# Kernel optimization log

Hardware: AMD Instinct MI355X
Metric: run time of the kernel (lower is better)

## Reference

```python
import jax, jax.numpy as jnp
import numpy as np
import math

CHANNELS = 512
N_HEADS = 8
K_CH = CHANNELS // N_HEADS            # 64 per-head dim
ROPE_D = int(K_CH * 0.5)              # 32 dims get RoPE, rest pass through
BASE = 10000


def _rope(x):
    # x: [b, h, t, dk]; rotate first ROPE_D dims (half-split style, matching the torch module)
    d = ROPE_D
    t = x.shape[2]
    theta = 1.0 / (BASE ** (jnp.arange(0, d, 2, dtype=jnp.float32) / d))      # [d/2]
    ang = jnp.arange(t, dtype=jnp.float32)[:, None] * theta[None, :]          # [t, d/2]
    ang = jnp.concatenate([ang, ang], axis=-1)                                # [t, d]
    cos = jnp.cos(ang)[None, None, :, :].astype(x.dtype)
    sin = jnp.sin(ang)[None, None, :, :].astype(x.dtype)
    x_rope, x_pass = x[..., :d], x[..., d:]
    neg_half = jnp.concatenate([-x_rope[..., d // 2:], x_rope[..., :d // 2]], axis=-1)
    return jnp.concatenate([x_rope * cos + neg_half * sin, x_pass], axis=-1)


def _split_heads(y):
    # [b, (h c), t] -> [b, h, t, c]
    b, _, t = y.shape
    return y.reshape(b, N_HEADS, K_CH, t).transpose(0, 1, 3, 2)


def setup_inputs() -> dict:
    key = jax.random.key(0)
    ks = jax.random.split(key, 10)
    B, T = 8, 1024
    w_scale = 1.0 / math.sqrt(CHANNELS)
    return {
        "x": jax.random.normal(ks[0], (B, CHANNELS, T), jnp.float32),
        "c": jax.random.normal(ks[1], (B, CHANNELS, T), jnp.float32),
        "Wq": jax.random.normal(ks[2], (CHANNELS, CHANNELS), jnp.float32) * w_scale,
        "bq": jax.random.normal(ks[3], (CHANNELS,), jnp.float32) * 0.02,
        "Wk": jax.random.normal(ks[4], (CHANNELS, CHANNELS), jnp.float32) * w_scale,
        "bk": jax.random.normal(ks[5], (CHANNELS,), jnp.float32) * 0.02,
        "Wv": jax.random.normal(ks[6], (CHANNELS, CHANNELS), jnp.float32) * w_scale,
        "bv": jax.random.normal(ks[7], (CHANNELS,), jnp.float32) * 0.02,
        "Wo": jax.random.normal(ks[8], (CHANNELS, CHANNELS), jnp.float32) * w_scale,
        "bo": jax.random.normal(ks[9], (CHANNELS,), jnp.float32) * 0.02,
    }


def reference(x, c, Wq, bq, Wk, bk, Wv, bv, Wo, bo):
    # 1x1 Conv1d == per-timestep linear over channels
    q = jnp.einsum('oc,bct->bot', Wq, x) + bq[None, :, None]
    k = jnp.einsum('oc,bct->bot', Wk, c) + bk[None, :, None]
    v = jnp.einsum('oc,bct->bot', Wv, c) + bv[None, :, None]

    q = _rope(_split_heads(q))            # [b,h,t,ck]
    k = _rope(_split_heads(k))            # [b,h,s,ck]
    v = _split_heads(v)                   # [b,h,s,ck]

    scale = 1.0 / math.sqrt(K_CH)
    scores = jnp.einsum('bhtc,bhsc->bhts', q, k) * scale
    p_attn = jax.nn.softmax(scores, axis=-1)       # dropout p=0 -> identity
    out = jnp.einsum('bhts,bhsc->bhtc', p_attn, v)

    b, _, t, _ = out.shape
    out = out.transpose(0, 1, 3, 2).reshape(b, CHANNELS, t)   # [b, (h c), t]
    return jnp.einsum('oc,bct->bot', Wo, out) + bo[None, :, None]
```

## Files before the change

kernel.cpp:

```cpp
#include <hip/hip_runtime.h>

typedef __bf16 bf16x8 __attribute__((ext_vector_type(8)));
typedef float  f32x4  __attribute__((ext_vector_type(4)));

__device__ __forceinline__ unsigned short f2bf(float f){
    union { float f; unsigned u; } v; v.f = f;
    v.u += 0x7fffu + ((v.u >> 16) & 1u);
    return (unsigned short)(v.u >> 16);
}
__device__ __forceinline__ unsigned short f2bf_trunc(float f){
    union { float f; unsigned u; } v; v.f = f;
    return (unsigned short)(v.u >> 16);
}
__device__ __forceinline__ void gl2lds16(const unsigned short* g, unsigned short* l){
    __builtin_amdgcn_global_load_lds(
        (const __attribute__((address_space(1))) void*)g,
        (__attribute__((address_space(3))) void*)l, 16, 0, 0);
}

__global__ __launch_bounds__(256) void transpose_cvt(const float* __restrict__ x, const float* __restrict__ c,
                                                     const float* __restrict__ w0, const float* __restrict__ w1,
                                                     const float* __restrict__ w2, const float* __restrict__ w3,
                                                     unsigned short* __restrict__ xt, unsigned short* __restrict__ ct,
                                                     unsigned short* __restrict__ o0, unsigned short* __restrict__ o1,
                                                     unsigned short* __restrict__ o2, unsigned short* __restrict__ o3){
    __shared__ float tile[64][72];
    const int z = blockIdx.z;
    if (z == 16){
        int fid = (blockIdx.x * 8 + blockIdx.y) * 256 + threadIdx.x;
        const float* in; unsigned short* out;
        switch (fid >> 13){
            case 0: in = w0; out = o0; break;
            case 1: in = w1; out = o1; break;
            case 2: in = w2; out = o2; break;
            default: in = w3; out = o3; break;
        }
        int off = (fid & 8191) * 32;
        #pragma unroll
        for (int j = 0; j < 8; j++){
            float4 v = *(const float4*)(in + off + j*4);
            ushort4 o; o.x = f2bf(v.x); o.y = f2bf(v.y); o.z = f2bf(v.z); o.w = f2bf(v.w);
            *(ushort4*)(out + off + j*4) = o;
        }
        return;
    }
    const float* in = (z < 8) ? x : c;
    unsigned short* out = (z < 8) ? xt : ct;
    const int b = z & 7;
    const int t0 = blockIdx.x * 64, c0 = blockIdx.y * 64;
    const int tid = threadIdx.x;
    {
        int r = tid >> 2, q = (tid & 3) * 16;
        const float* src = in + ((size_t)b * 512 + c0 + r) * 1024 + t0 + q;
        #pragma unroll
        for (int j = 0; j < 4; j++)
            *(float4*)&tile[r][q + j*4] = ((const float4*)src)[j];
    }
    __syncthreads();
    {
        int tr = tid >> 2, cj = (tid & 3) * 16;
        unsigned pw[8];
        #pragma unroll
        for (int j = 0; j < 8; j++){
            unsigned lo = f2bf(tile[cj + 2*j    ][tr]);
            unsigned hi = f2bf(tile[cj + 2*j + 1][tr]);
            pw[j] = lo | (hi << 16);
        }
        unsigned short* dst = out + ((size_t)b * 1024 + t0 + tr) * 512 + c0 + cj;
        uint4 q0 = {pw[0], pw[1], pw[2], pw[3]};
        uint4 q1 = {pw[4], pw[5], pw[6], pw[7]};
        ((uint4*)dst)[0] = q0;
        ((uint4*)dst)[1] = q1;
    }
}

__device__ __forceinline__ void gemm_mainloop(const unsigned short* __restrict__ A,
                                              const unsigned short* __restrict__ Bm,
                                              unsigned short* a_s, unsigned short* b_s,
                                              int m0, int n0, int tid, f32x4 acc[4][4]){
    const int wave = tid >> 6, lane = tid & 63;
    const int l15 = lane & 15, l4 = lane >> 4;
    const int mw = (wave >> 1) * 64, nw = (wave & 1) * 64;
    const int r8 = lane >> 3, c8l = lane & 7;
    const int csw = (c8l ^ r8) * 8;
    const int rp = l15 & 7;

    for (int k0 = 0; k0 < 512; k0 += 64){
        #pragma unroll
        for (int i = 0; i < 4; i++){
            int rg = i * 4 + wave;
            int row = rg * 8 + r8;
            gl2lds16(A  + (size_t)(m0 + row) * 512 + k0 + csw, a_s + rg * 512);
            gl2lds16(Bm + (size_t)(n0 + row) * 512 + k0 + csw, b_s + rg * 512);
        }
        __syncthreads();
        #pragma unroll
        for (int kk = 0; kk < 2; kk++){
            bf16x8 af[4], bfr[4];
            #pragma unroll
            for (int mt = 0; mt < 4; mt++)
                af[mt] = *(const bf16x8*)&a_s[(mw + mt*16 + l15)*64 + (((kk*4) + l4) ^ rp)*8];
            #pragma unroll
            for (int ct = 0; ct < 4; ct++)
                bfr[ct] = *(const bf16x8*)&b_s[(nw + ct*16 + l15)*64 + (((kk*4) + l4) ^ rp)*8];
            #pragma unroll
            for (int mt = 0; mt < 4; mt++)
                #pragma unroll
                for (int ct = 0; ct < 4; ct++)
                    acc[mt][ct] = __builtin_amdgcn_mfma_f32_16x16x32_bf16(
                        af[mt], bfr[ct], acc[mt][ct], 0, 0, 0);
        }
        __syncthreads();
    }
}

__global__ __launch_bounds__(256) void qkv_gemm(const unsigned short* __restrict__ xt,
                                                const unsigned short* __restrict__ ct,
                                                const unsigned short* __restrict__ wq,
                                                const unsigned short* __restrict__ wk,
                                                const unsigned short* __restrict__ wv,
                                                const float* __restrict__ bq_,
                                                const float* __restrict__ bk_,
                                                const float* __restrict__ bv_,
                                                unsigned short* __restrict__ qt,
                                                unsigned short* __restrict__ kt,
                                                unsigned short* __restrict__ vct){
    __shared__ unsigned short a_s[128*64];
    __shared__ unsigned short b_s[128*64];
    const int z = blockIdx.y, bid = blockIdx.x;
    const unsigned short *A, *Bm;
    int m0, n0;
    if (z == 0){ A = xt; Bm = wq; m0 = (bid >> 2)*128; n0 = (bid & 3)*128; }
    else if (z == 1){ A = ct; Bm = wk; m0 = (bid >> 2)*128; n0 = (bid & 3)*128; }
    else { A = wv; Bm = ct; m0 = (bid & 3)*128; n0 = (bid >> 2)*128; }
    const int tid = threadIdx.x;
    const int wave = tid >> 6, lane = tid & 63;
    const int l15 = lane & 15, l4 = lane >> 4;
    const int mw = (wave >> 1) * 64, nw = (wave & 1) * 64;
    const f32x4 vzero = {0.f, 0.f, 0.f, 0.f};
    f32x4 acc[4][4];
    #pragma unroll
    for (int i = 0; i < 4; i++)
        #pragma unroll
        for (int j = 0; j < 4; j++) acc[i][j] = vzero;

    gemm_mainloop(A, Bm, a_s, b_s, m0, n0, tid, acc);

    if (z < 2){
        unsigned short* out = (z == 0) ? qt : kt;
        const float* bias = (z == 0) ? bq_ : bk_;
        const float osc = (z == 0) ? 0.1803368801111137f : 1.0f;
        float bv4[4];
        #pragma unroll
        for (int ct2 = 0; ct2 < 4; ct2++) bv4[ct2] = bias[n0 + nw + ct2*16 + l15];
        const float theta = __powf(10000.0f, -(float)l15 * (1.0f / 16.0f));
        #pragma unroll
        for (int mt = 0; mt < 4; mt++){
            #pragma unroll
            for (int rr = 0; rr < 4; rr++){
                int row = m0 + mw + mt*16 + l4*4 + rr;
                int t = row & 1023;
                float v[4];
                #pragma unroll
                for (int ct2 = 0; ct2 < 4; ct2++) v[ct2] = acc[mt][ct2][rr] + bv4[ct2];
                float sn, cn;
                __sincosf((float)t * theta, &sn, &cn);
                float r0 = v[0] * cn - v[1] * sn;
                float r1 = v[1] * cn + v[0] * sn;
                v[0] = r0; v[1] = r1;
                #pragma unroll
                for (int ct2 = 0; ct2 < 4; ct2++)
                    out[(size_t)row * 512 + n0 + nw + ct2*16 + l15] = f2bf(v[ct2] * osc);
            }
        }
    } else {
        #pragma unroll
        for (int mt = 0; mt < 4; mt++){
            #pragma unroll
            for (int rr = 0; rr < 4; rr++){
                int row = m0 + mw + mt*16 + l4*4 + rr;
                float bb = bv_[row];
                #pragma unroll
                for (int ct2 = 0; ct2 < 4; ct2++){
                    int n = n0 + nw + ct2*16 + l15;
                    size_t oaddr = (size_t)(n >> 10) * 524288 + (size_t)row * 1024 + (n & 1023);
                    vct[oaddr] = f2bf(acc[mt][ct2][rr] + bb);
                }
            }
        }
    }
}

__global__ __launch_bounds__(256) void gemm_o(const unsigned short* __restrict__ wo,
                                              const unsigned short* __restrict__ attnT,
                                              const float* __restrict__ bo,
                                              float* __restrict__ out){
    __shared__ unsigned short a_s[64*64];
    __shared__ unsigned short b_s[128*64];
    const int m0 = blockIdx.x * 64, n0 = blockIdx.y * 128;
    const int tid = threadIdx.x;
    const int wave = tid >> 6, lane = tid & 63;
    const int l15 = lane & 15, l4 = lane >> 4;
    const int nw = wave * 32;
    const int r8 = lane >> 3, c8l = lane & 7;
    const int csw = (c8l ^ r8) * 8;
    const int rp = l15 & 7;
    const f32x4 vzero = {0.f, 0.f, 0.f, 0.f};
    f32x4 acc[4][2];
    #pragma unroll
    for (int i = 0; i < 4; i++){ acc[i][0] = vzero; acc[i][1] = vzero; }

    for (int k0 = 0; k0 < 512; k0 += 64){
        #pragma unroll
        for (int i = 0; i < 2; i++){
            int rg = wave * 2 + i;
            gl2lds16(wo + (size_t)(m0 + rg*8 + r8) * 512 + k0 + csw, a_s + rg * 512);
        }
        #pragma unroll
        for (int i = 0; i < 4; i++){
            int rg = wave * 4 + i;
            gl2lds16(attnT + (size_t)(n0 + rg*8 + r8) * 512 + k0 + csw, b_s + rg * 512);
        }
        __syncthreads();
        #pragma unroll
        for (int kk = 0; kk < 2; kk++){
            bf16x8 af[4], bfr[2];
            #pragma unroll
            for (int mt = 0; mt < 4; mt++)
                af[mt] = *(const bf16x8*)&a_s[(mt*16 + l15)*64 + (((kk*4) + l4) ^ rp)*8];
            #pragma unroll
            for (int ct = 0; ct < 2; ct++)
                bfr[ct] = *(const bf16x8*)&b_s[(nw + ct*16 + l15)*64 + (((kk*4) + l4) ^ rp)*8];
            #pragma unroll
            for (int mt = 0; mt < 4; mt++)
                #pragma unroll
                for (int ct = 0; ct < 2; ct++)
                    acc[mt][ct] = __builtin_amdgcn_mfma_f32_16x16x32_bf16(
                        af[mt], bfr[ct], acc[mt][ct], 0, 0, 0);
        }
        __syncthreads();
    }

    #pragma unroll
    for (int mt = 0; mt < 4; mt++){
        #pragma unroll
        for (int rr = 0; rr < 4; rr++){
            int row = m0 + mt*16 + l4*4 + rr;
            float bb = bo[row];
            #pragma unroll
            for (int ct2 = 0; ct2 < 2; ct2++){
                int n = n0 + nw + ct2*16 + l15;
                size_t oaddr = (size_t)(n >> 10) * 524288 + (size_t)row * 1024 + (n & 1023);
                out[oaddr] = acc[mt][ct2][rr] + bb;
            }
        }
    }
}

__global__ __launch_bounds__(256, 2) void flash_attn(const unsigned short* __restrict__ qt,
                                                     const unsigned short* __restrict__ kt,
                                                     const unsigned short* __restrict__ vct,
                                                     unsigned short* __restrict__ attnT){
    __shared__ unsigned short k_s[2][64*64];
    __shared__ unsigned short v_s[2][64*64];
    __shared__ unsigned short p_s[4][16*72];
    const int bhq = blockIdx.x;
    const int bh = bhq & 63, b = bh >> 3, h = bh & 7;
    const int q0 = (bhq >> 6) * 128;
    const int tid = threadIdx.x, wave = tid >> 6, lane = tid & 63;
    const int l15 = lane & 15, l4 = lane >> 4;
    const int r8 = lane >> 3, c8l = lane & 7;
    const int csw = (c8l ^ r8) * 8;
    const int rp = l15 & 7;
    const f32x4 vzero = {0.f, 0.f, 0.f, 0.f};
    const unsigned short* kbase = kt  + (size_t)(b*1024)*512 + h*64;
    const unsigned short* vbase = vct + (size_t)(b*512 + h*64)*1024;

    bf16x8 qf[2][2];
    #pragma unroll
    for (int st = 0; st < 2; st++)
        #pragma unroll
        for (int kh = 0; kh < 2; kh++)
            qf[st][kh] = *(const bf16x8*)(qt + (size_t)(b*1024 + q0 + wave*32 + st*16 + l15)*512
                                             + h*64 + kh*32 + l4*8);
    f32x4 o_acc[2][4], l_acc[2];
    #pragma unroll
    for (int st = 0; st < 2; st++){
        l_acc[st] = vzero;
        #pragma unroll
        for (int dt = 0; dt < 4; dt++) o_acc[st][dt] = vzero;
    }
    const __bf16 one_bf = (__bf16)1.0f;
    const bf16x8 ones = {one_bf, one_bf, one_bf, one_bf, one_bf, one_bf, one_bf, one_bf};

    auto stage = [&](int tile, int buf){
        const int s0n = tile * 64;
        #pragma unroll
        for (int i = 0; i < 2; i++){
            int rg = i * 4 + wave;
            int row = rg * 8 + r8;
            gl2lds16(kbase + (size_t)(s0n + row)*512 + csw, &k_s[buf][rg*512]);
            gl2lds16(vbase + (size_t)row*1024 + s0n + csw, &v_s[buf][rg*512]);
        }
    };
    stage(0, 0);
    __syncthreads();

    for (int it = 0; it < 16; ++it){
        const int cur = it & 1;
        if (it < 15) stage(it + 1, cur ^ 1);
        bf16x8 kf[2][4], vf[2][4];
        #pragma unroll
        for (int kh = 0; kh < 2; kh++)
            #pragma unroll
            for (int ct = 0; ct < 4; ct++)
                kf[kh][ct] = *(const bf16x8*)&k_s[cur][(ct*16 + l15)*64 + ((kh*4 + l4) ^ rp)*8];
        #pragma unroll
        for (int sh = 0; sh < 2; sh++)
            #pragma unroll
            for (int dt = 0; dt < 4; dt++)
                vf[sh][dt] = *(const bf16x8*)&v_s[cur][(dt*16 + l15)*64 + ((sh*4 + l4) ^ rp)*8];
        #pragma unroll
        for (int st = 0; st < 2; st++){
            f32x4 sa[4];
            #pragma unroll
            for (int ct = 0; ct < 4; ct++) sa[ct] = vzero;
            #pragma unroll
            for (int kh = 0; kh < 2; kh++)
                #pragma unroll
                for (int ct = 0; ct < 4; ct++)
                    sa[ct] = __builtin_amdgcn_mfma_f32_16x16x32_bf16(qf[st][kh], kf[kh][ct], sa[ct], 0, 0, 0);
            #pragma unroll
            for (int ct = 0; ct < 4; ct++)
                #pragma unroll
                for (int rr = 0; rr < 4; rr++)
                    sa[ct][rr] = exp2f(sa[ct][rr]);
            #pragma unroll
            for (int ct = 0; ct < 4; ct++)
                #pragma unroll
                for (int rr = 0; rr < 4; rr++)
                    p_s[wave][(l4*4 + rr)*72 + ct*16 + l15] = f2bf_trunc(sa[ct][rr]);
            bf16x8 ap0 = *(const bf16x8*)&p_s[wave][l15*72 + l4*8];
            bf16x8 ap1 = *(const bf16x8*)&p_s[wave][l15*72 + 32 + l4*8];
            l_acc[st] = __builtin_amdgcn_mfma_f32_16x16x32_bf16(ap0, ones, l_acc[st], 0, 0, 0);
            l_acc[st] = __builtin_amdgcn_mfma_f32_16x16x32_bf16(ap1, ones, l_acc[st], 0, 0, 0);
            #pragma unroll
            for (int dt = 0; dt < 4; dt++){
                o_acc[st][dt] = __builtin_amdgcn_mfma_f32_16x16x32_bf16(ap0, vf[0][dt], o_acc[st][dt], 0, 0, 0);
                o_acc[st][dt] = __builtin_amdgcn_mfma_f32_16x16x32_bf16(ap1, vf[1][dt], o_acc[st][dt], 0, 0, 0);
            }
        }
        __syncthreads();
    }
    #pragma unroll
    for (int st = 0; st < 2; st++){
        float rl[4];
        #pragma unroll
        for (int rr = 0; rr < 4; rr++) rl[rr] = __builtin_amdgcn_rcpf(l_acc[st][rr]);
        #pragma unroll
        for (int dt = 0; dt < 4; dt++)
            #pragma unroll
            for (int rr = 0; rr < 4; rr++){
                int row = q0 + wave*32 + st*16 + l4*4 + rr;
                attnT[(size_t)(b*1024 + row)*512 + h*64 + dt*16 + l15] = f2bf(o_acc[st][dt][rr] * rl[rr]);
            }
    }
}

extern "C" void kernel_launch(void* const* d_in, const int* in_sizes, int n_in,
                              void* d_out, int out_size, void* d_ws, size_t ws_size,
                              hipStream_t stream){
    const float* x  = (const float*)d_in[0];
    const float* c  = (const float*)d_in[1];
    const float* Wq = (const float*)d_in[2];
    const float* bq = (const float*)d_in[3];
    const float* Wk = (const float*)d_in[4];
    const float* bk = (const float*)d_in[5];
    const float* Wv = (const float*)d_in[6];
    const float* bv = (const float*)d_in[7];
    const float* Wo = (const float*)d_in[8];
    const float* bo = (const float*)d_in[9];

    unsigned short* wq_b = (unsigned short*)d_ws;
    unsigned short* wk_b = wq_b + 262144;
    unsigned short* wv_b = wk_b + 262144;
    unsigned short* wo_b = wv_b + 262144;
    unsigned short* xt   = wo_b + 262144;
    unsigned short* ct   = xt  + 4194304;
    unsigned short* qt   = ct  + 4194304;
    unsigned short* kt   = qt  + 4194304;
    unsigned short* vct  = kt  + 4194304;
    unsigned short* attnT = xt;

    transpose_cvt<<<dim3(16, 8, 17), 256, 0, stream>>>(x, c, Wq, Wk, Wv, Wo,
                                                       xt, ct, wq_b, wk_b, wv_b, wo_b);
    qkv_gemm<<<dim3(256, 3), 256, 0, stream>>>(xt, ct, wq_b, wk_b, wv_b, bq, bk, bv, qt, kt, vct);
    flash_attn<<<dim3(512), 256, 0, stream>>>(qt, kt, vct, attnT);
    gemm_o<<<dim3(8, 64), 256, 0, stream>>>(wo_b, attnT, bo, (float*)d_out);
}
```

Measured before the change: 171.4 us.

## Fuse all four stages into one cooperative persistent kernel with grid syncs

Merges the transpose/convert, QKV GEMM, flash attention and output GEMM into one cooperative kernel of 512 blocks that uses grid.sync between stages, with shared memory held in a union. The goal is to drop three kernel launch gaps and their tail drain. In exchange it takes on grid-wide barrier cost, a fixed grid of 512 blocks that loops over stage work (the QKV stage has 768 tiles, so some blocks take two), and a launch bound of 2 blocks per CU. The old four-kernel path stays as a fallback if the cooperative launch fails.

```diff
diff --git a/kernel.cpp b/kernel.cpp
--- a/kernel.cpp
+++ b/kernel.cpp
@@ -1,4 +1,6 @@
 #include <hip/hip_runtime.h>
+#include <hip/hip_cooperative_groups.h>
+namespace cg = cooperative_groups;
 
 typedef __bf16 bf16x8 __attribute__((ext_vector_type(8)));
 typedef float  f32x4  __attribute__((ext_vector_type(4)));
@@ -18,61 +20,9 @@
         (__attribute__((address_space(3))) void*)l, 16, 0, 0);
 }
 
-__global__ __launch_bounds__(256) void transpose_cvt(const float* __restrict__ x, const float* __restrict__ c,
-                                                     const float* __restrict__ w0, const float* __restrict__ w1,
-                                                     const float* __restrict__ w2, const float* __restrict__ w3,
-                                                     unsigned short* __restrict__ xt, unsigned short* __restrict__ ct,
-                                                     unsigned short* __restrict__ o0, unsigned short* __restrict__ o1,
-                                                     unsigned short* __restrict__ o2, unsigned short* __restrict__ o3){
-    __shared__ float tile[64][72];
-    const int z = blockIdx.z;
-    if (z == 16){
-        int fid = (blockIdx.x * 8 + blockIdx.y) * 256 + threadIdx.x;
-        const float* in; unsigned short* out;
-        switch (fid >> 13){
-            case 0: in = w0; out = o0; break;
-            case 1: in = w1; out = o1; break;
-            case 2: in = w2; out = o2; break;
-            default: in = w3; out = o3; break;
-        }
-        int off = (fid & 8191) * 32;
-        #pragma unroll
-        for (int j = 0; j < 8; j++){
-            float4 v = *(const float4*)(in + off + j*4);
-            ushort4 o; o.x = f2bf(v.x); o.y = f2bf(v.y); o.z = f2bf(v.z); o.w = f2bf(v.w);
-            *(ushort4*)(out + off + j*4) = o;
-        }
-        return;
-    }
-    const float* in = (z < 8) ? x : c;
-    unsigned short* out = (z < 8) ? xt : ct;
-    const int b = z & 7;
-    const int t0 = blockIdx.x * 64, c0 = blockIdx.y * 64;
-    const int tid = threadIdx.x;
-    {
-        int r = tid >> 2, q = (tid & 3) * 16;
-        const float* src = in + ((size_t)b * 512 + c0 + r) * 1024 + t0 + q;
-        #pragma unroll
-        for (int j = 0; j < 4; j++)
-            *(float4*)&tile[r][q + j*4] = ((const float4*)src)[j];
-    }
-    __syncthreads();
-    {
-        int tr = tid >> 2, cj = (tid & 3) * 16;
-        unsigned pw[8];
-        #pragma unroll
-        for (int j = 0; j < 8; j++){
-            unsigned lo = f2bf(tile[cj + 2*j    ][tr]);
-            unsigned hi = f2bf(tile[cj + 2*j + 1][tr]);
-            pw[j] = lo | (hi << 16);
-        }
-        unsigned short* dst = out + ((size_t)b * 1024 + t0 + tr) * 512 + c0 + cj;
-        uint4 q0 = {pw[0], pw[1], pw[2], pw[3]};
-        uint4 q1 = {pw[4], pw[5], pw[6], pw[7]};
-        ((uint4*)dst)[0] = q0;
-        ((uint4*)dst)[1] = q1;
-    }
-}
+struct SMemG { unsigned short a[128*64]; unsigned short b[128*64]; };
+struct SMemF { unsigned short k[2][64*64]; unsigned short v[2][64*64]; unsigned short p[4][16*72]; };
+union SMem { float tr[64*72]; SMemG g; SMemF f; };
 
 __device__ __forceinline__ void gemm_mainloop(const unsigned short* __restrict__ A,
                                               const unsigned short* __restrict__ Bm,
@@ -112,6 +62,340 @@
         }
         __syncthreads();
     }
+}
+
+__device__ __forceinline__ void qkv_tile(int z, int bid2,
+                                         const unsigned short* xt, const unsigned short* ct,
+                                         const unsigned short* wq, const unsigned short* wk,
+                                         const unsigned short* wv,
+                                         const float* bq_, const float* bk_, const float* bv_,
+                                         unsigned short* qt, unsigned short* kt, unsigned short* vct,
+                                         unsigned short* a_s, unsigned short* b_s, int tid){
+    const unsigned short *A, *Bm;
+    int m0, n0;
+    if (z == 0){ A = xt; Bm = wq; m0 = (bid2 >> 2)*128; n0 = (bid2 & 3)*128; }
+    else if (z == 1){ A = ct; Bm = wk; m0 = (bid2 >> 2)*128; n0 = (bid2 & 3)*128; }
+    else { A = wv; Bm = ct; m0 = (bid2 & 3)*128; n0 = (bid2 >> 2)*128; }
+    const int wave = tid >> 6, lane = tid & 63;
+    const int l15 = lane & 15, l4 = lane >> 4;
+    const int mw = (wave >> 1) * 64, nw = (wave & 1) * 64;
+    const f32x4 vzero = {0.f, 0.f, 0.f, 0.f};
+    f32x4 acc[4][4];
+    #pragma unroll
+    for (int i = 0; i < 4; i++)
+        #pragma unroll
+        for (int j = 0; j < 4; j++) acc[i][j] = vzero;
+
+    gemm_mainloop(A, Bm, a_s, b_s, m0, n0, tid, acc);
+
+    if (z < 2){
+        unsigned short* out = (z == 0) ? qt : kt;
+        const float* bias = (z == 0) ? bq_ : bk_;
+        const float osc = (z == 0) ? 0.1803368801111137f : 1.0f;
+        float bv4[4];
+        #pragma unroll
+        for (int ct2 = 0; ct2 < 4; ct2++) bv4[ct2] = bias[n0 + nw + ct2*16 + l15];
+        const float theta = __powf(10000.0f, -(float)l15 * (1.0f / 16.0f));
+        #pragma unroll
+        for (int mt = 0; mt < 4; mt++){
+            #pragma unroll
+            for (int rr = 0; rr < 4; rr++){
+                int row = m0 + mw + mt*16 + l4*4 + rr;
+                int t = row & 1023;
+                float v[4];
+                #pragma unroll
+                for (int ct2 = 0; ct2 < 4; ct2++) v[ct2] = acc[mt][ct2][rr] + bv4[ct2];
+                float sn, cn;
+                __sincosf((float)t * theta, &sn, &cn);
+                float r0 = v[0] * cn - v[1] * sn;
+                float r1 = v[1] * cn + v[0] * sn;
+                v[0] = r0; v[1] = r1;
+                #pragma unroll
+                for (int ct2 = 0; ct2 < 4; ct2++)
+                    out[(size_t)row * 512 + n0 + nw + ct2*16 + l15] = f2bf(v[ct2] * osc);
+            }
+        }
+    } else {
+        #pragma unroll
+        for (int mt = 0; mt < 4; mt++){
+            #pragma unroll
+            for (int rr = 0; rr < 4; rr++){
+                int row = m0 + mw + mt*16 + l4*4 + rr;
+                float bb = bv_[row];
+                #pragma unroll
+                for (int ct2 = 0; ct2 < 4; ct2++){
+                    int n = n0 + nw + ct2*16 + l15;
+                    size_t oaddr = (size_t)(n >> 10) * 524288 + (size_t)row * 1024 + (n & 1023);
+                    vct[oaddr] = f2bf(acc[mt][ct2][rr] + bb);
+                }
+            }
+        }
+    }
+}
+
+__device__ __forceinline__ void flash_tile(int b, int h, int q0,
+                                           const unsigned short* qt, const unsigned short* kt,
+                                           const unsigned short* vct, unsigned short* attnT,
+                                           SMemF* sf, int tid){
+    const int wave = tid >> 6, lane = tid & 63;
+    const int l15 = lane & 15, l4 = lane >> 4;
+    const int r8 = lane >> 3, c8l = lane & 7;
+    const int csw = (c8l ^ r8) * 8;
+    const int rp = l15 & 7;
+    const f32x4 vzero = {0.f, 0.f, 0.f, 0.f};
+    const unsigned short* kbase = kt  + (size_t)(b*1024)*512 + h*64;
+    const unsigned short* vbase = vct + (size_t)(b*512 + h*64)*1024;
+
+    bf16x8 qf[2][2];
+    #pragma unroll
+    for (int st = 0; st < 2; st++)
+        #pragma unroll
+        for (int kh = 0; kh < 2; kh++)
+            qf[st][kh] = *(const bf16x8*)(qt + (size_t)(b*1024 + q0 + wave*32 + st*16 + l15)*512
+                                             + h*64 + kh*32 + l4*8);
+    f32x4 o_acc[2][4], l_acc[2];
+    #pragma unroll
+    for (int st = 0; st < 2; st++){
+        l_acc[st] = vzero;
+        #pragma unroll
+        for (int dt = 0; dt < 4; dt++) o_acc[st][dt] = vzero;
+    }
+    const __bf16 one_bf = (__bf16)1.0f;
+    const bf16x8 ones = {one_bf, one_bf, one_bf, one_bf, one_bf, one_bf, one_bf, one_bf};
+
+    auto stage = [&](int tile, int buf){
+        const int s0n = tile * 64;
+        #pragma unroll
+        for (int i = 0; i < 2; i++){
+            int rg = i * 4 + wave;
+            int row = rg * 8 + r8;
+            gl2lds16(kbase + (size_t)(s0n + row)*512 + csw, &sf->k[buf][rg*512]);
+            gl2lds16(vbase + (size_t)row*1024 + s0n + csw, &sf->v[buf][rg*512]);
+        }
+    };
+    stage(0, 0);
+    __syncthreads();
+
+    for (int it = 0; it < 16; ++it){
+        const int cur = it & 1;
+        if (it < 15) stage(it + 1, cur ^ 1);
+        bf16x8 kf[2][4], vf[2][4];
+        #pragma unroll
+        for (int kh = 0; kh < 2; kh++)
+            #pragma unroll
+            for (int ct = 0; ct < 4; ct++)
+                kf[kh][ct] = *(const bf16x8*)&sf->k[cur][(ct*16 + l15)*64 + ((kh*4 + l4) ^ rp)*8];
+        #pragma unroll
+        for (int sh = 0; sh < 2; sh++)
+            #pragma unroll
+            for (int dt = 0; dt < 4; dt++)
+                vf[sh][dt] = *(const bf16x8*)&sf->v[cur][(dt*16 + l15)*64 + ((sh*4 + l4) ^ rp)*8];
+        #pragma unroll
+        for (int st = 0; st < 2; st++){
+            f32x4 sa[4];
+            #pragma unroll
+            for (int ct = 0; ct < 4; ct++) sa[ct] = vzero;
+            #pragma unroll
+            for (int kh = 0; kh < 2; kh++)
+                #pragma unroll
+                for (int ct = 0; ct < 4; ct++)
+                    sa[ct] = __builtin_amdgcn_mfma_f32_16x16x32_bf16(qf[st][kh], kf[kh][ct], sa[ct], 0, 0, 0);
+            #pragma unroll
+            for (int ct = 0; ct < 4; ct++)
+                #pragma unroll
+                for (int rr = 0; rr < 4; rr++)
+                    sa[ct][rr] = exp2f(sa[ct][rr]);
+            #pragma unroll
+            for (int ct = 0; ct < 4; ct++)
+                #pragma unroll
+                for (int rr = 0; rr < 4; rr++)
+                    sf->p[wave][(l4*4 + rr)*72 + ct*16 + l15] = f2bf_trunc(sa[ct][rr]);
+            bf16x8 ap0 = *(const bf16x8*)&sf->p[wave][l15*72 + l4*8];
+            bf16x8 ap1 = *(const bf16x8*)&sf->p[wave][l15*72 + 32 + l4*8];
+            l_acc[st] = __builtin_amdgcn_mfma_f32_16x16x32_bf16(ap0, ones, l_acc[st], 0, 0, 0);
+            l_acc[st] = __builtin_amdgcn_mfma_f32_16x16x32_bf16(ap1, ones, l_acc[st], 0, 0, 0);
+            #pragma unroll
+            for (int dt = 0; dt < 4; dt++){
+                o_acc[st][dt] = __builtin_amdgcn_mfma_f32_16x16x32_bf16(ap0, vf[0][dt], o_acc[st][dt], 0, 0, 0);
+                o_acc[st][dt] = __builtin_amdgcn_mfma_f32_16x16x32_bf16(ap1, vf[1][dt], o_acc[st][dt], 0, 0, 0);
+            }
+        }
+        __syncthreads();
+    }
+    #pragma unroll
+    for (int st = 0; st < 2; st++){
+        float rl[4];
+        #pragma unroll
+        for (int rr = 0; rr < 4; rr++) rl[rr] = __builtin_amdgcn_rcpf(l_acc[st][rr]);
+        #pragma unroll
+        for (int dt = 0; dt < 4; dt++)
+            #pragma unroll
+            for (int rr = 0; rr < 4; rr++){
+                int row = q0 + wave*32 + st*16 + l4*4 + rr;
+                attnT[(size_t)(b*1024 + row)*512 + h*64 + dt*16 + l15] = f2bf(o_acc[st][dt][rr] * rl[rr]);
+            }
+    }
+}
+
+__device__ __forceinline__ void gemmo_tile(int m0, int n0,
+                                           const unsigned short* wo, const unsigned short* attnT,
+                                           const float* bo, float* out,
+                                           unsigned short* a_s, unsigned short* b_s, int tid){
+    const int wave = tid >> 6, lane = tid & 63;
+    const int l15 = lane & 15, l4 = lane >> 4;
+    const int nw = wave * 32;
+    const int r8 = lane >> 3, c8l = lane & 7;
+    const int csw = (c8l ^ r8) * 8;
+    const int rp = l15 & 7;
+    const f32x4 vzero = {0.f, 0.f, 0.f, 0.f};
+    f32x4 acc[4][2];
+    #pragma unroll
+    for (int i = 0; i < 4; i++){ acc[i][0] = vzero; acc[i][1] = vzero; }
+
+    for (int k0 = 0; k0 < 512; k0 += 64){
+        #pragma unroll
+        for (int i = 0; i < 2; i++){
+            int rg = wave * 2 + i;
+            gl2lds16(wo + (size_t)(m0 + rg*8 + r8) * 512 + k0 + csw, a_s + rg * 512);
+        }
+        #pragma unroll
+        for (int i = 0; i < 4; i++){
+            int rg = wave * 4 + i;
+            gl2lds16(attnT + (size_t)(n0 + rg*8 + r8) * 512 + k0 + csw, b_s + rg * 512);
+        }
+        __syncthreads();
+        #pragma unroll
+        for (int kk = 0; kk < 2; kk++){
+            bf16x8 af[4], bfr[2];
+            #pragma unroll
+            for (int mt = 0; mt < 4; mt++)
+                af[mt] = *(const bf16x8*)&a_s[(mt*16 + l15)*64 + (((kk*4) + l4) ^ rp)*8];
+            #pragma unroll
+            for (int ct = 0; ct < 2; ct++)
+                bfr[ct] = *(const bf16x8*)&b_s[(nw + ct*16 + l15)*64 + (((kk*4) + l4) ^ rp)*8];
+            #pragma unroll
+            for (int mt = 0; mt < 4; mt++)
+                #pragma unroll
+                for (int ct = 0; ct < 2; ct++)
+                    acc[mt][ct] = __builtin_amdgcn_mfma_f32_16x16x32_bf16(
+                        af[mt], bfr[ct], acc[mt][ct], 0, 0, 0);
+        }
+        __syncthreads();
+    }
+
+    #pragma unroll
+    for (int mt = 0; mt < 4; mt++){
+        #pragma unroll
+        for (int rr = 0; rr < 4; rr++){
+            int row = m0 + mt*16 + l4*4 + rr;
+            float bb = bo[row];
+            #pragma unroll
+            for (int ct2 = 0; ct2 < 2; ct2++){
+                int n = n0 + nw + ct2*16 + l15;
+                size_t oaddr = (size_t)(n >> 10) * 524288 + (size_t)row * 1024 + (n & 1023);
+                out[oaddr] = acc[mt][ct2][rr] + bb;
+            }
+        }
+    }
+}
+
+__device__ __forceinline__ void transpose_unit(int u,
+        const float* x, const float* c, const float* w0, const float* w1,
+        const float* w2, const float* w3,
+        unsigned short* xt, unsigned short* ct,
+        unsigned short* o0, unsigned short* o1, unsigned short* o2, unsigned short* o3,
+        float* tr, int tid){
+    if (u >= 2048){
+        int fid = (u - 2048) * 256 + tid;
+        const float* in; unsigned short* out;
+        switch (fid >> 13){
+            case 0: in = w0; out = o0; break;
+            case 1: in = w1; out = o1; break;
+            case 2: in = w2; out = o2; break;
+            default: in = w3; out = o3; break;
+        }
+        int off = (fid & 8191) * 32;
+        #pragma unroll
+        for (int j = 0; j < 8; j++){
+            float4 v = *(const float4*)(in + off + j*4);
+            ushort4 o; o.x = f2bf(v.x); o.y = f2bf(v.y); o.z = f2bf(v.z); o.w = f2bf(v.w);
+            *(ushort4*)(out + off + j*4) = o;
+        }
+        return;
+    }
+    const int z = u >> 7, rem = u & 127;
+    const float* in = (z < 8) ? x : c;
+    unsigned short* out = (z < 8) ? xt : ct;
+    const int b = z & 7;
+    const int t0 = (rem >> 3) * 64, c0 = (rem & 7) * 64;
+    {
+        int r = tid >> 2, q = (tid & 3) * 16;
+        const float* src = in + ((size_t)b * 512 + c0 + r) * 1024 + t0 + q;
+        #pragma unroll
+        for (int j = 0; j < 4; j++)
+            *(float4*)&tr[r*72 + q + j*4] = ((const float4*)src)[j];
+    }
+    __syncthreads();
+    {
+        int trr = tid >> 2, cj = (tid & 3) * 16;
+        unsigned pw[8];
+        #pragma unroll
+        for (int j = 0; j < 8; j++){
+            unsigned lo = f2bf(tr[(cj + 2*j    )*72 + trr]);
+            unsigned hi = f2bf(tr[(cj + 2*j + 1)*72 + trr]);
+            pw[j] = lo | (hi << 16);
+        }
+        unsigned short* dst = out + ((size_t)b * 1024 + t0 + trr) * 512 + c0 + cj;
+        uint4 q0v = {pw[0], pw[1], pw[2], pw[3]};
+        uint4 q1v = {pw[4], pw[5], pw[6], pw[7]};
+        ((uint4*)dst)[0] = q0v;
+        ((uint4*)dst)[1] = q1v;
+    }
+    __syncthreads();
+}
+
+__global__ __launch_bounds__(256, 2) void mha_fused(
+        const float* __restrict__ x,  const float* __restrict__ c,
+        const float* __restrict__ Wq, const float* __restrict__ bq,
+        const float* __restrict__ Wk, const float* __restrict__ bk,
+        const float* __restrict__ Wv, const float* __restrict__ bv,
+        const float* __restrict__ Wo, const float* __restrict__ bo,
+        unsigned short* __restrict__ wq_b, unsigned short* __restrict__ wk_b,
+        unsigned short* __restrict__ wv_b, unsigned short* __restrict__ wo_b,
+        unsigned short* __restrict__ xt,  unsigned short* __restrict__ ct,
+        unsigned short* __restrict__ qt,  unsigned short* __restrict__ kt,
+        unsigned short* __restrict__ vct, float* __restrict__ out){
+    __shared__ SMem sm;
+    cg::grid_group grid = cg::this_grid();
+    const int bid = blockIdx.x, tid = threadIdx.x;
+    unsigned short* attnT = xt;
+
+    for (int u = bid; u < 2176; u += 512)
+        transpose_unit(u, x, c, Wq, Wk, Wv, Wo, xt, ct, wq_b, wk_b, wv_b, wo_b, sm.tr, tid);
+    grid.sync();
+
+    for (int u = bid; u < 768; u += 512)
+        qkv_tile(u >> 8, u & 255, xt, ct, wq_b, wk_b, wv_b, bq, bk, bv,
+                 qt, kt, vct, sm.g.a, sm.g.b, tid);
+    grid.sync();
+
+    flash_tile((bid & 63) >> 3, bid & 7, (bid >> 6) * 128, qt, kt, vct, attnT, &sm.f, tid);
+    grid.sync();
+
+    gemmo_tile((bid & 7) * 64, (bid >> 3) * 128, wo_b, attnT, bo, out, sm.g.a, sm.g.b, tid);
+}
+
+__global__ __launch_bounds__(256) void transpose_cvt(const float* __restrict__ x, const float* __restrict__ c,
+                                                     const float* __restrict__ w0, const float* __restrict__ w1,
+                                                     const float* __restrict__ w2, const float* __restrict__ w3,
+                                                     unsigned short* __restrict__ xt, unsigned short* __restrict__ ct,
+                                                     unsigned short* __restrict__ o0, unsigned short* __restrict__ o1,
+                                                     unsigned short* __restrict__ o2, unsigned short* __restrict__ o3){
+    __shared__ float tile[64*72];
+    const int z = blockIdx.z;
+    int u = (z == 16) ? 2048 + blockIdx.x * 8 + blockIdx.y
+                      : z * 128 + blockIdx.x * 8 + blockIdx.y;
+    transpose_unit(u, x, c, w0, w1, w2, w3, xt, ct, o0, o1, o2, o3, tile, threadIdx.x);
 }
 
 __global__ __launch_bounds__(256) void qkv_gemm(const unsigned short* __restrict__ xt,
@@ -125,246 +409,26 @@
                                                 unsigned short* __restrict__ qt,
                                                 unsigned short* __restrict__ kt,
                                                 unsigned short* __restrict__ vct){
-    __shared__ unsigned short a_s[128*64];
-    __shared__ unsigned short b_s[128*64];
-    const int z = blockIdx.y, bid = blockIdx.x;
-    const unsigned short *A, *Bm;
-    int m0, n0;
-    if (z == 0){ A = xt; Bm = wq; m0 = (bid >> 2)*128; n0 = (bid & 3)*128; }
-    else if (z == 1){ A = ct; Bm = wk; m0 = (bid >> 2)*128; n0 = (bid & 3)*128; }
-    else { A = wv; Bm = ct; m0 = (bid & 3)*128; n0 = (bid >> 2)*128; }
-    const int tid = threadIdx.x;
-    const int wave = tid >> 6, lane = tid & 63;
-    const int l15 = lane & 15, l4 = lane >> 4;
-    const int mw = (wave >> 1) * 64, nw = (wave & 1) * 64;
-    const f32x4 vzero = {0.f, 0.f, 0.f, 0.f};
-    f32x4 acc[4][4];
-    #pragma unroll
-    for (int i = 0; i < 4; i++)
-        #pragma unroll
-        for (int j = 0; j < 4; j++) acc[i][j] = vzero;
-
-    gemm_mainloop(A, Bm, a_s, b_s, m0, n0, tid, acc);
-
-    if (z < 2){
-        unsigned short* out = (z == 0) ? qt : kt;
-        const float* bias = (z == 0) ? bq_ : bk_;
-        const float osc = (z == 0) ? 0.1803368801111137f : 1.0f;
-        float bv4[4];
-        #pragma unroll
-        for (int ct2 = 0; ct2 < 4; ct2++) bv4[ct2] = bias[n0 + nw + ct2*16 + l15];
-        const float theta = __powf(10000.0f, -(float)l15 * (1.0f / 16.0f));
-        #pragma unroll
-        for (int mt = 0; mt < 4; mt++){
-            #pragma unroll
-            for (int rr = 0; rr < 4; rr++){
-                int row = m0 + mw + mt*16 + l4*4 + rr;
-                int t = row & 1023;
-                float v[4];
-                #pragma unroll
-                for (int ct2 = 0; ct2 < 4; ct2++) v[ct2] = acc[mt][ct2][rr] + bv4[ct2];
-                float sn, cn;
-                __sincosf((float)t * theta, &sn, &cn);
-                float r0 = v[0] * cn - v[1] * sn;
-                float r1 = v[1] * cn + v[0] * sn;
-                v[0] = r0; v[1] = r1;
-                #pragma unroll
-                for (int ct2 = 0; ct2 < 4; ct2++)
-                    out[(size_t)row * 512 + n0 + nw + ct2*16 + l15] = f2bf(v[ct2] * osc);
-            }
-        }
-    } else {
-        #pragma unroll
-        for (int mt = 0; mt < 4; mt++){
-            #pragma unroll
-            for (int rr = 0; rr < 4; rr++){
-                int row = m0 + mw + mt*16 + l4*4 + rr;
-                float bb = bv_[row];
-                #pragma unroll
-                for (int ct2 = 0; ct2 < 4; ct2++){
-                    int n = n0 + nw + ct2*16 + l15;
-                    size_t oaddr = (size_t)(n >> 10) * 524288 + (size_t)row * 1024 + (n & 1023);
-                    vct[oaddr] = f2bf(acc[mt][ct2][rr] + bb);
-                }
-            }
-        }
-    }
+    __shared__ SMemG sg;
+    qkv_tile(blockIdx.y, blockIdx.x, xt, ct, wq, wk, wv, bq_, bk_, bv_,
+             qt, kt, vct, sg.a, sg.b, threadIdx.x);
+}
+
+__global__ __launch_bounds__(256, 2) void flash_attn(const unsigned short* __restrict__ qt,
+                                                     const unsigned short* __restrict__ kt,
+                                                     const unsigned short* __restrict__ vct,
+                                                     unsigned short* __restrict__ attnT){
+    __shared__ SMemF sf;
+    const int bhq = blockIdx.x;
+    flash_tile((bhq & 63) >> 3, bhq & 7, (bhq >> 6) * 128, qt, kt, vct, attnT, &sf, threadIdx.x);
 }
 
 __global__ __launch_bounds__(256) void gemm_o(const unsigned short* __restrict__ wo,
                                               const unsigned short* __restrict__ attnT,
                                               const float* __restrict__ bo,
                                               float* __restrict__ out){
-    __shared__ unsigned short a_s[64*64];
-    __shared__ unsigned short b_s[128*64];
-    const int m0 = blockIdx.x * 64, n0 = blockIdx.y * 128;
-    const int tid = threadIdx.x;
-    const int wave = tid >> 6, lane = tid & 63;
-    const int l15 = lane & 15, l4 = lane >> 4;
-    const int nw = wave * 32;
-    const int r8 = lane >> 3, c8l = lane & 7;
-    const int csw = (c8l ^ r8) * 8;
-    const int rp = l15 & 7;
-    const f32x4 vzero = {0.f, 0.f, 0.f, 0.f};
-    f32x4 acc[4][2];
-    #pragma unroll
-    for (int i = 0; i < 4; i++){ acc[i][0] = vzero; acc[i][1] = vzero; }
-
-    for (int k0 = 0; k0 < 512; k0 += 64){
-        #pragma unroll
-        for (int i = 0; i < 2; i++){
-            int rg = wave * 2 + i;
-            gl2lds16(wo + (size_t)(m0 + rg*8 + r8) * 512 + k0 + csw, a_s + rg * 512);
-        }
-        #pragma unroll
-        for (int i = 0; i < 4; i++){
-            int rg = wave * 4 + i;
-            gl2lds16(attnT + (size_t)(n0 + rg*8 + r8) * 512 + k0 + csw, b_s + rg * 512);
-        }
-        __syncthreads();
-        #pragma unroll
-        for (int kk = 0; kk < 2; kk++){
-            bf16x8 af[4], bfr[2];
-            #pragma unroll
-            for (int mt = 0; mt < 4; mt++)
-                af[mt] = *(const bf16x8*)&a_s[(mt*16 + l15)*64 + (((kk*4) + l4) ^ rp)*8];
-            #pragma unroll
-            for (int ct = 0; ct < 2; ct++)
-                bfr[ct] = *(const bf16x8*)&b_s[(nw + ct*16 + l15)*64 + (((kk*4) + l4) ^ rp)*8];
-            #pragma unroll
-            for (int mt = 0; mt < 4; mt++)
-                #pragma unroll
-                for (int ct = 0; ct < 2; ct++)
-                    acc[mt][ct] = __builtin_amdgcn_mfma_f32_16x16x32_bf16(
-                        af[mt], bfr[ct], acc[mt][ct], 0, 0, 0);
-        }
-        __syncthreads();
-    }
-
-    #pragma unroll
-    for (int mt = 0; mt < 4; mt++){
-        #pragma unroll
-        for (int rr = 0; rr < 4; rr++){
-            int row = m0 + mt*16 + l4*4 + rr;
-            float bb = bo[row];
-            #pragma unroll
-            for (int ct2 = 0; ct2 < 2; ct2++){
-                int n = n0 + nw + ct2*16 + l15;
-                size_t oaddr = (size_t)(n >> 10) * 524288 + (size_t)row * 1024 + (n & 1023);
-                out[oaddr] = acc[mt][ct2][rr] + bb;
-            }
-        }
-    }
-}
-
-__global__ __launch_bounds__(256, 2) void flash_attn(const unsigned short* __restrict__ qt,
-                                                     const unsigned short* __restrict__ kt,
-                                                     const unsigned short* __restrict__ vct,
-                                                     unsigned short* __restrict__ attnT){
-    __shared__ unsigned short k_s[2][64*64];
-    __shared__ unsigned short v_s[2][64*64];
-    __shared__ unsigned short p_s[4][16*72];
-    const int bhq = blockIdx.x;
-    const int bh = bhq & 63, b = bh >> 3, h = bh & 7;
-    const int q0 = (bhq >> 6) * 128;
-    const int tid = threadIdx.x, wave = tid >> 6, lane = tid & 63;
-    const int l15 = lane & 15, l4 = lane >> 4;
-    const int r8 = lane >> 3, c8l = lane & 7;
-    const int csw = (c8l ^ r8) * 8;
-    const int rp = l15 & 7;
-    const f32x4 vzero = {0.f, 0.f, 0.f, 0.f};
-    const unsigned short* kbase = kt  + (size_t)(b*1024)*512 + h*64;
-    const unsigned short* vbase = vct + (size_t)(b*512 + h*64)*1024;
-
-    bf16x8 qf[2][2];
-    #pragma unroll
-    for (int st = 0; st < 2; st++)
-        #pragma unroll
-        for (int kh = 0; kh < 2; kh++)
-            qf[st][kh] = *(const bf16x8*)(qt + (size_t)(b*1024 + q0 + wave*32 + st*16 + l15)*512
-                                             + h*64 + kh*32 + l4*8);
-    f32x4 o_acc[2][4], l_acc[2];
-    #pragma unroll
-    for (int st = 0; st < 2; st++){
-        l_acc[st] = vzero;
-        #pragma unroll
-        for (int dt = 0; dt < 4; dt++) o_acc[st][dt] = vzero;
-    }
-    const __bf16 one_bf = (__bf16)1.0f;
-    const bf16x8 ones = {one_bf, one_bf, one_bf, one_bf, one_bf, one_bf, one_bf, one_bf};
-
-    auto stage = [&](int tile, int buf){
-        const int s0n = tile * 64;
-        #pragma unroll
-        for (int i = 0; i < 2; i++){
-            int rg = i * 4 + wave;
-            int row = rg * 8 + r8;
-            gl2lds16(kbase + (size_t)(s0n + row)*512 + csw, &k_s[buf][rg*512]);
-            gl2lds16(vbase + (size_t)row*1024 + s0n + csw, &v_s[buf][rg*512]);
-        }
-    };
-    stage(0, 0);
-    __syncthreads();
-
-    for (int it = 0; it < 16; ++it){
-        const int cur = it & 1;
-        if (it < 15) stage(it + 1, cur ^ 1);
-        bf16x8 kf[2][4], vf[2][4];
-        #pragma unroll
-        for (int kh = 0; kh < 2; kh++)
-            #pragma unroll
-            for (int ct = 0; ct < 4; ct++)
-                kf[kh][ct] = *(const bf16x8*)&k_s[cur][(ct*16 + l15)*64 + ((kh*4 + l4) ^ rp)*8];
-        #pragma unroll
-        for (int sh = 0; sh < 2; sh++)
-            #pragma unroll
-            for (int dt = 0; dt < 4; dt++)
-                vf[sh][dt] = *(const bf16x8*)&v_s[cur][(dt*16 + l15)*64 + ((sh*4 + l4) ^ rp)*8];
-        #pragma unroll
-        for (int st = 0; st < 2; st++){
-            f32x4 sa[4];
-            #pragma unroll
-            for (int ct = 0; ct < 4; ct++) sa[ct] = vzero;
-            #pragma unroll
-            for (int kh = 0; kh < 2; kh++)
-                #pragma unroll
-                for (int ct = 0; ct < 4; ct++)
-                    sa[ct] = __builtin_amdgcn_mfma_f32_16x16x32_bf16(qf[st][kh], kf[kh][ct], sa[ct], 0, 0, 0);
-            #pragma unroll
-            for (int ct = 0; ct < 4; ct++)
-                #pragma unroll
-                for (int rr = 0; rr < 4; rr++)
-                    sa[ct][rr] = exp2f(sa[ct][rr]);
-            #pragma unroll
-            for (int ct = 0; ct < 4; ct++)
-                #pragma unroll
-                for (int rr = 0; rr < 4; rr++)
-                    p_s[wave][(l4*4 + rr)*72 + ct*16 + l15] = f2bf_trunc(sa[ct][rr]);
-            bf16x8 ap0 = *(const bf16x8*)&p_s[wave][l15*72 + l4*8];
-            bf16x8 ap1 = *(const bf16x8*)&p_s[wave][l15*72 + 32 + l4*8];
-            l_acc[st] = __builtin_amdgcn_mfma_f32_16x16x32_bf16(ap0, ones, l_acc[st], 0, 0, 0);
-            l_acc[st] = __builtin_amdgcn_mfma_f32_16x16x32_bf16(ap1, ones, l_acc[st], 0, 0, 0);
-            #pragma unroll
-            for (int dt = 0; dt < 4; dt++){
-                o_acc[st][dt] = __builtin_amdgcn_mfma_f32_16x16x32_bf16(ap0, vf[0][dt], o_acc[st][dt], 0, 0, 0);
-                o_acc[st][dt] = __builtin_amdgcn_mfma_f32_16x16x32_bf16(ap1, vf[1][dt], o_acc[st][dt], 0, 0, 0);
-            }
-        }
-        __syncthreads();
-    }
-    #pragma unroll
-    for (int st = 0; st < 2; st++){
-        float rl[4];
-        #pragma unroll
-        for (int rr = 0; rr < 4; rr++) rl[rr] = __builtin_amdgcn_rcpf(l_acc[st][rr]);
-        #pragma unroll
-        for (int dt = 0; dt < 4; dt++)
-            #pragma unroll
-            for (int rr = 0; rr < 4; rr++){
-                int row = q0 + wave*32 + st*16 + l4*4 + rr;
-                attnT[(size_t)(b*1024 + row)*512 + h*64 + dt*16 + l15] = f2bf(o_acc[st][dt][rr] * rl[rr]);
-            }
-    }
+    __shared__ SMemG sg;
+    gemmo_tile(blockIdx.x * 64, blockIdx.y * 128, wo, attnT, bo, out, sg.a, sg.b, threadIdx.x);
 }
 
 extern "C" void kernel_launch(void* const* d_in, const int* in_sizes, int n_in,
@@ -390,11 +454,20 @@
     unsigned short* qt   = ct  + 4194304;
     unsigned short* kt   = qt  + 4194304;
     unsigned short* vct  = kt  + 4194304;
-    unsigned short* attnT = xt;
-
-    transpose_cvt<<<dim3(16, 8, 17), 256, 0, stream>>>(x, c, Wq, Wk, Wv, Wo,
-                                                       xt, ct, wq_b, wk_b, wv_b, wo_b);
-    qkv_gemm<<<dim3(256, 3), 256, 0, stream>>>(xt, ct, wq_b, wk_b, wv_b, bq, bk, bv, qt, kt, vct);
-    flash_attn<<<dim3(512), 256, 0, stream>>>(qt, kt, vct, attnT);
-    gemm_o<<<dim3(8, 64), 256, 0, stream>>>(wo_b, attnT, bo, (float*)d_out);
-}
+    float* outf = (float*)d_out;
+
+    void* args[] = { (void*)&x, (void*)&c, (void*)&Wq, (void*)&bq, (void*)&Wk, (void*)&bk,
+                     (void*)&Wv, (void*)&bv, (void*)&Wo, (void*)&bo,
+                     (void*)&wq_b, (void*)&wk_b, (void*)&wv_b, (void*)&wo_b,
+                     (void*)&xt, (void*)&ct, (void*)&qt, (void*)&kt, (void*)&vct, (void*)&outf };
+    hipError_t err = hipLaunchCooperativeKernel((const void*)mha_fused, dim3(512), dim3(256),
+                                                args, 0, stream);
+    if (err != hipSuccess){
+        unsigned short* attnT = xt;
+        transpose_cvt<<<dim3(16, 8, 17), 256, 0, stream>>>(x, c, Wq, Wk, Wv, Wo,
+                                                           xt, ct, wq_b, wk_b, wv_b, wo_b);
+        qkv_gemm<<<dim3(256, 3), 256, 0, stream>>>(xt, ct, wq_b, wk_b, wv_b, bq, bk, bv, qt, kt, vct);
+        flash_attn<<<dim3(512), 256, 0, stream>>>(qt, kt, vct, attnT);
+        gemm_o<<<dim3(8, 64), 256, 0, stream>>>(wo_b, attnT, bo, (float*)d_out);
+    }
+}
```

Measured after the change: 408.3 us. 138% more time.
